# Optimization experiments

Hardware: AMD Instinct MI355X
Metric: run time of the kernel (lower is better)

## Reference

```python
import jax, jax.numpy as jnp
import numpy as np

NUM_CLASSES = 64


def setup_inputs() -> dict:
    key = jax.random.key(0)
    k1, k2, k3, k4, k5 = jax.random.split(key, 5)
    N, D = 65536, 256
    return {
        "src_feat": jax.random.normal(k1, (N, D), dtype=jnp.float32),
        "trg_feat": jax.random.normal(k2, (N, D), dtype=jnp.float32),
        "src_label": jax.random.randint(k3, (N,), 0, NUM_CLASSES, dtype=jnp.int64),
        "trg_label": jax.random.randint(k4, (N,), 0, NUM_CLASSES, dtype=jnp.int64),
        "trg_feat_un": jax.random.normal(k5, (N, D), dtype=jnp.float32),
    }


def _kl_mean(p_logits, q_logits):
    # torch F.kl_div(log_softmax(p), softmax(q), reduction='mean')
    # = mean over ALL elements of q * (log q - log_softmax(p))
    q = jax.nn.softmax(q_logits, axis=-1)
    logq = jax.nn.log_softmax(q_logits, axis=-1)
    logp = jax.nn.log_softmax(p_logits, axis=-1)
    return jnp.mean(q * (logq - logp))


def reference(src_feat, trg_feat, src_label, trg_label, trg_feat_un):
    C = NUM_CLASSES
    ones_s = jnp.ones(src_feat.shape[0], dtype=src_feat.dtype)
    ones_t = jnp.ones(trg_feat.shape[0], dtype=trg_feat.dtype)
    sum_s = jax.ops.segment_sum(src_feat, src_label, num_segments=C)  # [C,D]
    sum_t = jax.ops.segment_sum(trg_feat, trg_label, num_segments=C)  # [C,D]
    cnt_s = jax.ops.segment_sum(ones_s, src_label, num_segments=C)    # [C]
    cnt_t = jax.ops.segment_sum(ones_t, trg_label, num_segments=C)    # [C]
    u_s = sum_s / cnt_s[:, None]
    u_t = sum_t / cnt_t[:, None]
    u_st = (sum_s + sum_t) / (cnt_s + cnt_t)[:, None]

    feats = jnp.concatenate((src_feat, trg_feat), axis=0)  # [2N, D]
    P_s = feats @ u_s.T    # [2N, C]
    P_t = feats @ u_t.T
    P_st = feats @ u_st.T

    loss_st = (_kl_mean(P_s, P_t) + _kl_mean(P_t, P_s)) / 2
    loss_sst = (_kl_mean(P_s, P_st) + _kl_mean(P_st, P_s)) / 2
    loss_tst = (_kl_mean(P_t, P_st) + _kl_mean(P_st, P_t)) / 2
    return (loss_st + loss_sst + loss_tst) / 3
```

## Files before the change

### kernel.cpp

```cpp
#include <hip/hip_runtime.h>

#define N_ROWS 65536
#define DIMS 256
#define NCLS 64

#define P_SUM_S 0
#define P_SUM_T 131072
#define P_CNT_S 262144
#define P_CNT_T 262400
#define ACC_OFF 262656
#define DONE_OFF 262784
#define RECIP_OFF 262788
#define BPACK_OFF 262992
#define BF16A_OFF 279376
#define ZERO_FLOATS 262788

typedef __attribute__((ext_vector_type(8))) short bf16x8;
typedef __attribute__((ext_vector_type(4))) float f32x4;

__device__ __forceinline__ short f2bf(float f) {
  unsigned u = __float_as_uint(f);
  u += 0x7fffu + ((u >> 16) & 1u);
  return (short)(u >> 16);
}

__device__ __forceinline__ float wave_sum64(float v) {
#pragma unroll
  for (int m = 32; m > 0; m >>= 1) v += __shfl_xor(v, m, 64);
  return v;
}
__device__ __forceinline__ double wave_sum64d(double v) {
#pragma unroll
  for (int m = 32; m > 0; m >>= 1) v += __shfl_xor(v, m, 64);
  return v;
}
__device__ __forceinline__ float seg_max16(float v) {
#pragma unroll
  for (int m = 8; m > 0; m >>= 1) v = fmaxf(v, __shfl_xor(v, m, 64));
  return v;
}
__device__ __forceinline__ float seg_sum16(float v) {
#pragma unroll
  for (int m = 8; m > 0; m >>= 1) v += __shfl_xor(v, m, 64);
  return v;
}

__device__ __forceinline__ void gld16(const void* g, void* l) {
  __builtin_amdgcn_global_load_lds(
      (const __attribute__((address_space(1))) unsigned int*)g,
      (__attribute__((address_space(3))) unsigned int*)l, 16, 0, 0);
}

__global__ __launch_bounds__(256) void seg_sum_kernel(
    const float* __restrict__ src_feat, const float* __restrict__ trg_feat,
    const int* __restrict__ src_label, const int* __restrict__ trg_label,
    float* __restrict__ ws_f) {
  __shared__ float lsum[NCLS * DIMS];
  const int tid = threadIdx.x;
  const bool is_trg = blockIdx.x >= 256;
  const int blk = is_trg ? (blockIdx.x - 256) : blockIdx.x;
  const int part = blockIdx.x & 7;
  const int part4 = blockIdx.x & 3;
  const float* feat = is_trg ? trg_feat : src_feat;
  const int* label = is_trg ? trg_label : src_label;
  float* gsum = ws_f + (is_trg ? P_SUM_T : P_SUM_S) + part * 16384;
  float* gcnt = ws_f + (is_trg ? P_CNT_T : P_CNT_S) + part4 * 64;
  unsigned short* bfA = (unsigned short*)(ws_f + BF16A_OFF);
  const size_t grow0 = (size_t)(is_trg ? N_ROWS : 0) + (size_t)blk * 256;

  for (int i = tid; i < NCLS * DIMS; i += 256) lsum[i] = 0.f;
  __syncthreads();

  const int row0 = blk * 256;
  float cnt_local = 0.f;
  for (int r = 0; r < 256; r += 8) {
    int lb[8];
    float v[8];
#pragma unroll
    for (int i = 0; i < 8; ++i) {
      lb[i] = label[row0 + r + i];
      v[i] = feat[(size_t)(row0 + r + i) * DIMS + tid];
    }
#pragma unroll
    for (int i = 0; i < 8; ++i)
      bfA[(grow0 + r + i) * DIMS + tid] = (unsigned short)f2bf(v[i]);
#pragma unroll
    for (int i = 0; i < 8; ++i) {
      lsum[lb[i] * DIMS + tid] += v[i];
      if (tid < NCLS) cnt_local += (lb[i] == tid) ? 1.f : 0.f;
    }
  }
  __syncthreads();
  for (int c = 0; c < NCLS; ++c)
    atomicAdd(&gsum[c * DIMS + tid], lsum[c * DIMS + tid]);
  if (tid < NCLS) atomicAdd(&gcnt[tid], cnt_local);
}

__global__ __launch_bounds__(64) void pack_kernel(float* __restrict__ ws_f) {
  const int bx = blockIdx.x;
  const int s = bx >> 3;
  const int mt = bx & 7;
  const int mat = mt >> 2;
  const int tile = mt & 3;
  const int lane = threadIdx.x;
  const int c = tile * 16 + (lane & 15);

  if (s == 0 && mat == 0 && lane < 16) {
    float cs = 0.f, ct = 0.f;
#pragma unroll
    for (int p = 0; p < 4; ++p) {
      cs += ws_f[P_CNT_S + p * 64 + c];
      ct += ws_f[P_CNT_T + p * 64 + c];
    }
    ws_f[RECIP_OFF + c] = 1.f / cs;
    ws_f[RECIP_OFF + 64 + c] = 1.f / ct;
    ws_f[RECIP_OFF + 128 + c] = 1.f / (cs + ct);
  }

  const float* sb = ws_f + (mat ? P_SUM_T : P_SUM_S) + c * DIMS;
  const int k0 = s * 32 + (lane >> 4) * 8;
  float a8[8];
#pragma unroll
  for (int j = 0; j < 8; ++j) a8[j] = 0.f;
#pragma unroll
  for (int p = 0; p < 8; ++p) {
    const float4 lo = *(const float4*)(sb + p * 16384 + k0);
    const float4 hi = *(const float4*)(sb + p * 16384 + k0 + 4);
    a8[0] += lo.x; a8[1] += lo.y; a8[2] += lo.z; a8[3] += lo.w;
    a8[4] += hi.x; a8[5] += hi.y; a8[6] += hi.z; a8[7] += hi.w;
  }
  bf16x8 v;
#pragma unroll
  for (int j = 0; j < 8; ++j) v[j] = f2bf(a8[j]);
  ((bf16x8*)(ws_f + BPACK_OFF))[bx * 64 + lane] = v;
}

__global__ __launch_bounds__(256, 4) void main_kernel(
    const float* __restrict__ ws_f, double* __restrict__ acc,
    unsigned* __restrict__ done, float* __restrict__ out) {
  __shared__ unsigned short abuf[2][4096];
  __shared__ unsigned short bbuf[2][4096];
  __shared__ double wsum[4];
  __shared__ unsigned lastflag;

  const int tid = threadIdx.x;
  const int w = tid >> 6;
  const int lane = tid & 63;
  const int row0 = blockIdx.x * 128;
  const unsigned short* bfA = (const unsigned short*)(ws_f + BF16A_OFF);
  const unsigned short* bpk = (const unsigned short*)(ws_f + BPACK_OFF);

  const unsigned short* pa0 =
      bfA + (size_t)(row0 + w * 32 + (lane >> 2)) * DIMS +
      (((lane & 3) ^ ((lane >> 2) & 3)) * 8);
  const unsigned short* pa1 = pa0 + 16 * DIMS;
  const unsigned short* pb0 = bpk + (size_t)(w * 128 + lane) * 8;
  const unsigned short* pb1 = pb0 + 512;

#define STAGE(ss, bb)                                         \
  {                                                           \
    gld16(pa0 + (ss) * 32, &abuf[bb][w * 1024]);              \
    gld16(pa1 + (ss) * 32, &abuf[bb][w * 1024 + 512]);        \
    gld16(pb0 + (ss) * 4096, &bbuf[bb][w * 1024]);            \
    gld16(pb1 + (ss) * 4096, &bbuf[bb][w * 1024 + 512]);      \
  }

  float rs[4], rt[4], rst[4];
#pragma unroll
  for (int t = 0; t < 4; ++t) {
    const int c = t * 16 + (lane & 15);
    rs[t] = ws_f[RECIP_OFF + c];
    rt[t] = ws_f[RECIP_OFF + 64 + c];
    rst[t] = ws_f[RECIP_OFF + 128 + c];
  }

  f32x4 C[2][4][2];
#pragma unroll
  for (int m = 0; m < 2; ++m)
#pragma unroll
    for (int t = 0; t < 4; ++t)
#pragma unroll
      for (int g = 0; g < 2; ++g) C[m][t][g] = (f32x4){0.f, 0.f, 0.f, 0.f};

  STAGE(0, 0);
  __syncthreads();

  const int abase =
      (w * 32 + (lane & 15)) * 32 + (((lane >> 4) ^ (lane & 3)) * 8);

#pragma unroll
  for (int s = 0; s < 8; ++s) {
    const int cb = s & 1;
    if (s < 7) STAGE(s + 1, cb ^ 1);
    const bf16x8 a0 = *(const bf16x8*)&abuf[cb][abase];
    const bf16x8 a1 = *(const bf16x8*)&abuf[cb][abase + 512];
#pragma unroll
    for (int mt = 0; mt < 8; ++mt) {
      const bf16x8 b = *(const bf16x8*)&bbuf[cb][(mt * 64 + lane) * 8];
      C[mt >> 2][mt & 3][0] = __builtin_amdgcn_mfma_f32_16x16x32_bf16(
          a0, b, C[mt >> 2][mt & 3][0], 0, 0, 0);
      C[mt >> 2][mt & 3][1] = __builtin_amdgcn_mfma_f32_16x16x32_bf16(
          a1, b, C[mt >> 2][mt & 3][1], 0, 0, 0);
    }
    __syncthreads();
  }
#undef STAGE

  float total = 0.f;
#pragma unroll
  for (int g = 0; g < 2; ++g) {
#pragma unroll
    for (int r = 0; r < 4; ++r) {
      float va[4], vb[4], vc[4];
#pragma unroll
      for (int t = 0; t < 4; ++t) {
        const float gs = C[0][t][g][r];
        const float gt = C[1][t][g][r];
        va[t] = gs * rs[t];
        vb[t] = gt * rt[t];
        vc[t] = (gs + gt) * rst[t];
      }
      float ma = fmaxf(fmaxf(va[0], va[1]), fmaxf(va[2], va[3]));
      float mb = fmaxf(fmaxf(vb[0], vb[1]), fmaxf(vb[2], vb[3]));
      float mc = fmaxf(fmaxf(vc[0], vc[1]), fmaxf(vc[2], vc[3]));
      ma = seg_max16(ma); mb = seg_max16(mb); mc = seg_max16(mc);
      float ea[4], eb[4], ec[4];
      float sa = 0.f, sb = 0.f, sc = 0.f;
#pragma unroll
      for (int t = 0; t < 4; ++t) {
        ea[t] = __expf(va[t] - ma); sa += ea[t];
        eb[t] = __expf(vb[t] - mb); sb += eb[t];
        ec[t] = __expf(vc[t] - mc); sc += ec[t];
      }
      sa = seg_sum16(sa); sb = seg_sum16(sb); sc = seg_sum16(sc);
      const float La = ma + __logf(sa);
      const float Lb = mb + __logf(sb);
      const float Lc = mc + __logf(sc);
      const float isa = 1.f / sa, isb = 1.f / sb, isc = 1.f / sc;
#pragma unroll
      for (int t = 0; t < 4; ++t) {
        const float la = va[t] - La, lb = vb[t] - Lb, lc = vc[t] - Lc;
        const float pa = ea[t] * isa, pb = eb[t] * isb, pc = ec[t] * isc;
        total += pa * ((la - lb) + (la - lc)) + pb * ((lb - la) + (lb - lc)) +
                 pc * ((lc - la) + (lc - lb));
      }
    }
  }
  total = wave_sum64(total);
  if (lane == 0) wsum[w] = (double)total;
  __syncthreads();

  if (tid == 0) {
    const double bt = wsum[0] + wsum[1] + wsum[2] + wsum[3];
    atomicAdd(&acc[blockIdx.x & 63], bt);
    __threadfence();
    lastflag = (atomicAdd(done, 1u) == gridDim.x - 1) ? 1u : 0u;
  }
  __syncthreads();
  if (lastflag && tid < 64) {
    double v = atomicAdd(&acc[tid], 0.0);
    v = wave_sum64d(v);
    if (tid == 0) out[0] = (float)(v / 50331648.0);
  }
}

extern "C" void kernel_launch(void* const* d_in, const int* in_sizes, int n_in,
                              void* d_out, int out_size, void* d_ws, size_t ws_size,
                              hipStream_t stream) {
  const float* src_feat = (const float*)d_in[0];
  const float* trg_feat = (const float*)d_in[1];
  const int* src_label = (const int*)d_in[2];
  const int* trg_label = (const int*)d_in[3];
  float* ws_f = (float*)d_ws;
  double* acc = (double*)(ws_f + ACC_OFF);
  unsigned* done = (unsigned*)(ws_f + DONE_OFF);
  float* out = (float*)d_out;

  hipMemsetAsync(d_ws, 0, (size_t)ZERO_FLOATS * sizeof(float), stream);

  seg_sum_kernel<<<512, 256, 0, stream>>>(src_feat, trg_feat, src_label,
                                          trg_label, ws_f);
  pack_kernel<<<64, 64, 0, stream>>>(ws_f);
  main_kernel<<<1024, 256, 0, stream>>>(ws_f, acc, done, out);
}
```

Baseline: 252.7 us.

## Vectorize segment-sum loads with float4, software-prefetch rows, use LDS atomics

The segment-sum kernel now assigns each wave a separate row and has each lane read four consecutive floats with float4 loads. The next 8-row chunk is prefetched into registers while the current one is processed. bf16 copies are written as 4-element vectors. Because different waves can hit the same class at the same time, per-class accumulation switches to LDS atomicAdd, and the LDS layout is permuted so the final global atomics index it correctly. This trades more register pressure and contended LDS atomics for fewer, wider, better-overlapped global memory transactions.

```diff
diff --git a/kernel.cpp b/kernel.cpp
--- a/kernel.cpp
+++ b/kernel.cpp
@@ -17,6 +17,7 @@
 
 typedef __attribute__((ext_vector_type(8))) short bf16x8;
 typedef __attribute__((ext_vector_type(4))) float f32x4;
+typedef __attribute__((ext_vector_type(4))) unsigned short u16x4;
 
 __device__ __forceinline__ short f2bf(float f) {
   unsigned u = __float_as_uint(f);
@@ -57,6 +58,8 @@
     float* __restrict__ ws_f) {
   __shared__ float lsum[NCLS * DIMS];
   const int tid = threadIdx.x;
+  const int w = tid >> 6;
+  const int lane = tid & 63;
   const bool is_trg = blockIdx.x >= 256;
   const int blk = is_trg ? (blockIdx.x - 256) : blockIdx.x;
   const int part = blockIdx.x & 7;
@@ -68,32 +71,63 @@
   unsigned short* bfA = (unsigned short*)(ws_f + BF16A_OFF);
   const size_t grow0 = (size_t)(is_trg ? N_ROWS : 0) + (size_t)blk * 256;
 
-  for (int i = tid; i < NCLS * DIMS; i += 256) lsum[i] = 0.f;
+  {
+    f32x4* lz = (f32x4*)lsum;
+    for (int i = tid; i < NCLS * DIMS / 4; i += 256)
+      lz[i] = (f32x4){0.f, 0.f, 0.f, 0.f};
+  }
   __syncthreads();
 
   const int row0 = blk * 256;
+  const float* fbase = feat + (size_t)row0 * DIMS + lane * 4;
   float cnt_local = 0.f;
-  for (int r = 0; r < 256; r += 8) {
-    int lb[8];
-    float v[8];
+
+  float4 cur[8];
+  int lb[8];
+#define LOADCH(buf, lbuf, c)                                              \
+  {                                                                       \
+    _Pragma("unroll") for (int i = 0; i < 8; ++i) {                       \
+      const int idx = (c) * 8 + i;                                        \
+      lbuf[i] = label[row0 + idx * 4 + w];                                \
+      buf[i] = *(const float4*)(fbase + (size_t)(idx * 4 + w) * DIMS);    \
+    }                                                                     \
+  }
+
+  LOADCH(cur, lb, 0);
+  for (int c = 0; c < 8; ++c) {
+    float4 nxt[8];
+    int lbn[8];
+    if (c < 7) LOADCH(nxt, lbn, c + 1);
 #pragma unroll
     for (int i = 0; i < 8; ++i) {
-      lb[i] = label[row0 + r + i];
-      v[i] = feat[(size_t)(row0 + r + i) * DIMS + tid];
-    }
-#pragma unroll
-    for (int i = 0; i < 8; ++i)
-      bfA[(grow0 + r + i) * DIMS + tid] = (unsigned short)f2bf(v[i]);
+      const int idx = c * 8 + i;
+      const size_t grow = grow0 + idx * 4 + w;
+      u16x4 o;
+      o[0] = (unsigned short)f2bf(cur[i].x);
+      o[1] = (unsigned short)f2bf(cur[i].y);
+      o[2] = (unsigned short)f2bf(cur[i].z);
+      o[3] = (unsigned short)f2bf(cur[i].w);
+      *(u16x4*)(bfA + grow * DIMS + lane * 4) = o;
+      const int cls = lb[i];
+      atomicAdd(&lsum[cls * 256 + 0 * 64 + lane], cur[i].x);
+      atomicAdd(&lsum[cls * 256 + 1 * 64 + lane], cur[i].y);
+      atomicAdd(&lsum[cls * 256 + 2 * 64 + lane], cur[i].z);
+      atomicAdd(&lsum[cls * 256 + 3 * 64 + lane], cur[i].w);
+      cnt_local += (cls == lane) ? 1.f : 0.f;
+    }
 #pragma unroll
     for (int i = 0; i < 8; ++i) {
-      lsum[lb[i] * DIMS + tid] += v[i];
-      if (tid < NCLS) cnt_local += (lb[i] == tid) ? 1.f : 0.f;
-    }
-  }
-  __syncthreads();
-  for (int c = 0; c < NCLS; ++c)
-    atomicAdd(&gsum[c * DIMS + tid], lsum[c * DIMS + tid]);
-  if (tid < NCLS) atomicAdd(&gcnt[tid], cnt_local);
+      cur[i] = nxt[i];
+      lb[i] = lbn[i];
+    }
+  }
+#undef LOADCH
+  __syncthreads();
+
+  const int ild = (tid & 3) * 64 + (tid >> 2);
+  for (int cc = 0; cc < NCLS; ++cc)
+    atomicAdd(&gsum[cc * DIMS + tid], lsum[cc * 256 + ild]);
+  atomicAdd(&gcnt[lane], cnt_local);
 }
 
 __global__ __launch_bounds__(64) void pack_kernel(float* __restrict__ ws_f) {
```

Result: slower. 365.6 us (+44.7%).

## Split segment-sum blocks across feature quarters to shrink LDS and raise occupancy

Applied to the files above, without the earlier changes.

The segment-sum kernel now launches four times as many blocks. Each block covers 256 rows and one 64-wide quarter of the feature dimension, with each of its four waves handling 64 rows. The per-block LDS accumulator shrinks from 64 KB to 16 KB, so more blocks can be resident per CU to better hide global-memory latency. Because waves now share accumulator slots, updates use LDS atomics, and labels are broadcast with shuffles instead of repeated loads. This adds LDS atomic contention, while the total number of global atomic flushes stays the same.

```diff
diff --git a/kernel.cpp b/kernel.cpp
--- a/kernel.cpp
+++ b/kernel.cpp
@@ -51,49 +51,59 @@
       (__attribute__((address_space(3))) unsigned int*)l, 16, 0, 0);
 }
 
-__global__ __launch_bounds__(256) void seg_sum_kernel(
+__global__ __launch_bounds__(256, 8) void seg_sum_kernel(
     const float* __restrict__ src_feat, const float* __restrict__ trg_feat,
     const int* __restrict__ src_label, const int* __restrict__ trg_label,
     float* __restrict__ ws_f) {
-  __shared__ float lsum[NCLS * DIMS];
+  __shared__ float lsum[NCLS * 64];
+  __shared__ float lcnt[NCLS];
   const int tid = threadIdx.x;
-  const bool is_trg = blockIdx.x >= 256;
-  const int blk = is_trg ? (blockIdx.x - 256) : blockIdx.x;
-  const int part = blockIdx.x & 7;
-  const int part4 = blockIdx.x & 3;
+  const int lane = tid & 63;
+  const int w = tid >> 6;
+  const int bid = blockIdx.x;
+  const bool is_trg = bid >= 1024;
+  const int b = bid & 1023;
+  const int rowgrp = b >> 2;
+  const int dq = b & 3;
+  const int part = b & 7;
   const float* feat = is_trg ? trg_feat : src_feat;
   const int* label = is_trg ? trg_label : src_label;
   float* gsum = ws_f + (is_trg ? P_SUM_T : P_SUM_S) + part * 16384;
-  float* gcnt = ws_f + (is_trg ? P_CNT_T : P_CNT_S) + part4 * 64;
+  float* gcnt = ws_f + (is_trg ? P_CNT_T : P_CNT_S) + ((b >> 3) & 3) * 64;
   unsigned short* bfA = (unsigned short*)(ws_f + BF16A_OFF);
-  const size_t grow0 = (size_t)(is_trg ? N_ROWS : 0) + (size_t)blk * 256;
-
-  for (int i = tid; i < NCLS * DIMS; i += 256) lsum[i] = 0.f;
-  __syncthreads();
-
-  const int row0 = blk * 256;
-  float cnt_local = 0.f;
-  for (int r = 0; r < 256; r += 8) {
-    int lb[8];
+
+  const int d = dq * 64 + lane;
+  const int row0 = rowgrp * 256 + w * 64;
+  const size_t grow0 = (size_t)(is_trg ? N_ROWS : 0) + row0;
+
+  for (int i = tid; i < NCLS * 64; i += 256) lsum[i] = 0.f;
+  if (tid < NCLS) lcnt[tid] = 0.f;
+  __syncthreads();
+
+  const int lab = label[row0 + lane];
+  if (dq == 0) atomicAdd(&lcnt[lab], 1.f);
+
+  const float* fb = feat + (size_t)row0 * DIMS + d;
+  unsigned short* ob = bfA + grow0 * DIMS + d;
+
+  for (int c = 0; c < 8; ++c) {
     float v[8];
 #pragma unroll
+    for (int i = 0; i < 8; ++i) v[i] = fb[(size_t)(c * 8 + i) * DIMS];
+#pragma unroll
     for (int i = 0; i < 8; ++i) {
-      lb[i] = label[row0 + r + i];
-      v[i] = feat[(size_t)(row0 + r + i) * DIMS + tid];
-    }
-#pragma unroll
-    for (int i = 0; i < 8; ++i)
-      bfA[(grow0 + r + i) * DIMS + tid] = (unsigned short)f2bf(v[i]);
-#pragma unroll
-    for (int i = 0; i < 8; ++i) {
-      lsum[lb[i] * DIMS + tid] += v[i];
-      if (tid < NCLS) cnt_local += (lb[i] == tid) ? 1.f : 0.f;
-    }
-  }
-  __syncthreads();
-  for (int c = 0; c < NCLS; ++c)
-    atomicAdd(&gsum[c * DIMS + tid], lsum[c * DIMS + tid]);
-  if (tid < NCLS) atomicAdd(&gcnt[tid], cnt_local);
+      const int r = c * 8 + i;
+      ob[(size_t)r * DIMS] = (unsigned short)f2bf(v[i]);
+      const int cls = __shfl(lab, r, 64);
+      atomicAdd(&lsum[cls * 64 + lane], v[i]);
+    }
+  }
+  __syncthreads();
+
+  const int c0 = w * 16;
+  for (int cc = c0; cc < c0 + 16; ++cc)
+    atomicAdd(&gsum[cc * DIMS + d], lsum[cc * 64 + lane]);
+  if (dq == 0 && tid < NCLS) atomicAdd(&gcnt[tid], lcnt[tid]);
 }
 
 __global__ __launch_bounds__(64) void pack_kernel(float* __restrict__ ws_f) {
@@ -278,8 +288,8 @@
 
   hipMemsetAsync(d_ws, 0, (size_t)ZERO_FLOATS * sizeof(float), stream);
 
-  seg_sum_kernel<<<512, 256, 0, stream>>>(src_feat, trg_feat, src_label,
-                                          trg_label, ws_f);
+  seg_sum_kernel<<<2048, 256, 0, stream>>>(src_feat, trg_feat, src_label,
+                                           trg_label, ws_f);
   pack_kernel<<<64, 64, 0, stream>>>(ws_f);
   main_kernel<<<1024, 256, 0, stream>>>(ws_f, acc, done, out);
 }
```

Measured after the change: 350.9 us. +38.8%, slower.

## Software-pipeline segment-sum loads and stage labels in LDS

Applied to the files above, without the earlier changes.

The segment-sum kernel now stages each block's 256 labels in shared memory once and zeroes the shared accumulator with vector stores. Its row loop is restructured into 16-row chunks, with the next chunk's features prefetched into registers while the current chunk is converted to bf16 and accumulated. Shared-memory accumulation switches from read-modify-write to LDS atomicAdd, which removes the per-row load-dependency chain. The trade-off is higher register pressure from the double buffer, and atomic adds may cost more per operation than plain adds.

```diff
diff --git a/kernel.cpp b/kernel.cpp
--- a/kernel.cpp
+++ b/kernel.cpp
@@ -56,6 +56,7 @@
     const int* __restrict__ src_label, const int* __restrict__ trg_label,
     float* __restrict__ ws_f) {
   __shared__ float lsum[NCLS * DIMS];
+  __shared__ int llab[256];
   const int tid = threadIdx.x;
   const bool is_trg = blockIdx.x >= 256;
   const int blk = is_trg ? (blockIdx.x - 256) : blockIdx.x;
@@ -66,33 +67,56 @@
   float* gsum = ws_f + (is_trg ? P_SUM_T : P_SUM_S) + part * 16384;
   float* gcnt = ws_f + (is_trg ? P_CNT_T : P_CNT_S) + part4 * 64;
   unsigned short* bfA = (unsigned short*)(ws_f + BF16A_OFF);
-  const size_t grow0 = (size_t)(is_trg ? N_ROWS : 0) + (size_t)blk * 256;
-
-  for (int i = tid; i < NCLS * DIMS; i += 256) lsum[i] = 0.f;
-  __syncthreads();
 
   const int row0 = blk * 256;
+  const size_t grow0 = (size_t)(is_trg ? N_ROWS : 0) + row0;
+
+  {
+    f32x4* lz = (f32x4*)lsum;
+    for (int i = tid; i < NCLS * DIMS / 4; i += 256)
+      lz[i] = (f32x4){0.f, 0.f, 0.f, 0.f};
+  }
+  llab[tid] = label[row0 + tid];
+  __syncthreads();
+
+  const float* fcol = feat + (size_t)row0 * DIMS + tid;
+  unsigned short* ocol = bfA + grow0 * DIMS + tid;
   float cnt_local = 0.f;
-  for (int r = 0; r < 256; r += 8) {
-    int lb[8];
-    float v[8];
-#pragma unroll
-    for (int i = 0; i < 8; ++i) {
-      lb[i] = label[row0 + r + i];
-      v[i] = feat[(size_t)(row0 + r + i) * DIMS + tid];
-    }
-#pragma unroll
-    for (int i = 0; i < 8; ++i)
-      bfA[(grow0 + r + i) * DIMS + tid] = (unsigned short)f2bf(v[i]);
-#pragma unroll
-    for (int i = 0; i < 8; ++i) {
-      lsum[lb[i] * DIMS + tid] += v[i];
-      if (tid < NCLS) cnt_local += (lb[i] == tid) ? 1.f : 0.f;
-    }
-  }
-  __syncthreads();
-  for (int c = 0; c < NCLS; ++c)
-    atomicAdd(&gsum[c * DIMS + tid], lsum[c * DIMS + tid]);
+
+  float cur[16];
+  int lb[16];
+#define LOADCH(vbuf, lbuf, c)                                \
+  {                                                          \
+    _Pragma("unroll") for (int i = 0; i < 16; ++i) {         \
+      const int r = (c) * 16 + i;                            \
+      lbuf[i] = llab[r];                                     \
+      vbuf[i] = fcol[(size_t)r * DIMS];                      \
+    }                                                        \
+  }
+
+  LOADCH(cur, lb, 0);
+  for (int c = 0; c < 16; ++c) {
+    float nxt[16];
+    int lbn[16];
+    if (c < 15) LOADCH(nxt, lbn, c + 1);
+#pragma unroll
+    for (int i = 0; i < 16; ++i) {
+      const int r = c * 16 + i;
+      ocol[(size_t)r * DIMS] = (unsigned short)f2bf(cur[i]);
+      atomicAdd(&lsum[lb[i] * DIMS + tid], cur[i]);
+      cnt_local += (lb[i] == tid) ? 1.f : 0.f;
+    }
+#pragma unroll
+    for (int i = 0; i < 16; ++i) {
+      cur[i] = nxt[i];
+      lb[i] = lbn[i];
+    }
+  }
+#undef LOADCH
+  __syncthreads();
+
+  for (int cc = 0; cc < NCLS; ++cc)
+    atomicAdd(&gsum[cc * DIMS + tid], lsum[cc * DIMS + tid]);
   if (tid < NCLS) atomicAdd(&gcnt[tid], cnt_local);
 }
 
```

Measured after the change: 357.1 us. 1.41x slower.
